# Kernel optimization log

Hardware: AMD Instinct MI355X
Metric: run time of the kernel (lower is better)

The kernel has to match this reference:

```python
import jax, jax.numpy as jnp
import numpy as np
from jax import lax

B, FC, TC, HID, HR, G, H, W = 4, 64, 64, 48, 2, 8, 128, 256
D = 2 * HR + 1          # 5 disparity offsets
CG = FC // G            # channels per correlation group
GRU_IN = TC + 2 * FC + 4 + G * D  # 236


def conv2d(x, w, b=None, pad=0):
    y = lax.conv_general_dilated(x, w, (1, 1), [(pad, pad), (pad, pad)],
                                 dimension_numbers=('NCHW', 'OIHW', 'NCHW'))
    return y if b is None else y + b[None, :, None, None]


def group_norm(x, scale, bias, groups=8, eps=1e-5):
    Bn, C, Hh, Ww = x.shape
    xg = x.reshape(Bn, groups, -1)
    m = jnp.mean(xg, -1, keepdims=True)
    v = jnp.var(xg, -1, keepdims=True)
    xg = (xg - m) * lax.rsqrt(v + eps)
    return xg.reshape(Bn, C, Hh, Ww) * scale[None, :, None, None] + bias[None, :, None, None]


def hsample(f, x):
    """grid_sample(align_corners=True, padding_mode='border') specialized to
    horizontal-only displacement: gy hits exact rows so only width is interpolated.
    f: [B,C,H,W], x: [B,H,W] source x-coords (unnormalized)."""
    Wf = f.shape[-1]
    xc = jnp.clip(x, 0.0, Wf - 1)          # border padding clamps coordinate
    x0 = jnp.floor(xc)
    w1 = xc - x0
    i0 = x0.astype(jnp.int32)
    i1 = jnp.minimum(i0 + 1, Wf - 1)
    i0b = jnp.broadcast_to(i0[:, None], f.shape)
    i1b = jnp.broadcast_to(i1[:, None], f.shape)
    f0 = jnp.take_along_axis(f, i0b, axis=-1)
    f1 = jnp.take_along_axis(f, i1b, axis=-1)
    return f0 * (1.0 - w1)[:, None] + f1 * w1[:, None]


def _forward(d, sx, sy, conf, feat, fL, fR,
             conv_z_w, conv_z_b, conv_r_w, conv_r_b, conv_q_w, conv_q_b,
             trunk1_w, gn1_s, gn1_b, trunk2_w, gn2_s, gn2_b,
             head_d_w, head_d_b, head_sx_w, head_sx_b,
             head_sy_w, head_sy_b, head_conf_w, head_conf_b):
    Bn, C, Hh, Ww = fL.shape
    xx = jnp.arange(Ww, dtype=fL.dtype)
    d0 = d[:, 0]                                     # [B,H,W]

    # horizontal warp of right features at current disparity
    fR_w = hsample(fR, xx[None, None, :] - d0)       # [B,C,H,W]

    # correlation lookup over D offsets around d (vectorized over D)
    d_off = jnp.arange(D, dtype=fL.dtype) - HR       # [D]
    xs = xx[None, None, None, :] - (d0[:, None] + d_off[None, :, None, None])  # [B,D,H,W]
    samp = jax.vmap(lambda xd: hsample(fR, xd), in_axes=1, out_axes=1)(xs)     # [B,D,C,H,W]
    fL_g = fL.reshape(Bn, G, CG, Hh, Ww)
    fR_g = samp.reshape(Bn, D, G, CG, Hh, Ww)
    cost = jnp.einsum('bgchw,bdgchw->bgdhw', fL_g, fR_g) / CG  # mean over cg
    cost = cost.reshape(Bn, G * D, Hh, Ww)

    ctx = jnp.concatenate([fL, fR_w, d, sx, sy, conf, cost], axis=1)
    hctx = jnp.concatenate([feat, ctx], axis=1)
    z = jax.nn.sigmoid(conv2d(hctx, conv_z_w, conv_z_b, pad=1))
    r = jax.nn.sigmoid(conv2d(hctx, conv_r_w, conv_r_b, pad=1))
    q = jnp.tanh(conv2d(jnp.concatenate([r * feat, ctx], axis=1), conv_q_w, conv_q_b, pad=1))
    h_new = (1.0 - z) * feat + z * q

    t = jax.nn.silu(group_norm(conv2d(h_new, trunk1_w, pad=1), gn1_s, gn1_b))
    t = jax.nn.silu(group_norm(conv2d(t, trunk2_w, pad=1), gn2_s, gn2_b))

    d_out = jax.nn.softplus(conv2d(t, head_d_w, head_d_b) + d)
    sx_out = sx + conv2d(t, head_sx_w, head_sx_b) * 0.1
    sy_out = sy + conv2d(t, head_sy_w, head_sy_b) * 0.1
    conf_out = jax.nn.sigmoid(conv2d(t, head_conf_w, head_conf_b) + 2.0 * conf - 1.0)
    return d_out, sx_out, sy_out, h_new, conf_out


def setup_inputs() -> dict:
    key = jax.random.key(0)
    ks = jax.random.split(key, 24)
    s = 0.02  # weight scale so gates/tanh stay in sensitive range
    return {
        'd': jax.random.uniform(ks[0], (B, 1, H, W), jnp.float32) * 32.0,
        'sx': jax.random.normal(ks[1], (B, 1, H, W), jnp.float32) * 0.1,
        'sy': jax.random.normal(ks[2], (B, 1, H, W), jnp.float32) * 0.1,
        'conf': jax.random.uniform(ks[3], (B, 1, H, W), jnp.float32),
        'feat': jax.random.normal(ks[4], (B, TC, H, W), jnp.float32),
        'fL': jax.random.normal(ks[5], (B, FC, H, W), jnp.float32),
        'fR': jax.random.normal(ks[6], (B, FC, H, W), jnp.float32),
        'conv_z_w': jax.random.normal(ks[7], (TC, GRU_IN, 3, 3), jnp.float32) * s,
        'conv_z_b': jnp.zeros((TC,), jnp.float32),
        'conv_r_w': jax.random.normal(ks[8], (TC, GRU_IN, 3, 3), jnp.float32) * s,
        'conv_r_b': jnp.zeros((TC,), jnp.float32),
        'conv_q_w': jax.random.normal(ks[9], (TC, GRU_IN, 3, 3), jnp.float32) * s,
        'conv_q_b': jnp.zeros((TC,), jnp.float32),
        'trunk1_w': jax.random.normal(ks[10], (HID, TC, 3, 3), jnp.float32) * s,
        'gn1_s': jnp.ones((HID,), jnp.float32),
        'gn1_b': jnp.zeros((HID,), jnp.float32),
        'trunk2_w': jax.random.normal(ks[11], (HID, HID, 3, 3), jnp.float32) * s,
        'gn2_s': jnp.ones((HID,), jnp.float32),
        'gn2_b': jnp.zeros((HID,), jnp.float32),
        'head_d_w': jax.random.normal(ks[12], (1, HID, 1, 1), jnp.float32) * s,
        'head_d_b': jnp.zeros((1,), jnp.float32),
        'head_sx_w': jax.random.normal(ks[13], (1, HID, 1, 1), jnp.float32) * s,
        'head_sx_b': jnp.zeros((1,), jnp.float32),
        'head_sy_w': jax.random.normal(ks[14], (1, HID, 1, 1), jnp.float32) * s,
        'head_sy_b': jnp.zeros((1,), jnp.float32),
        'head_conf_w': jax.random.normal(ks[15], (1, HID, 1, 1), jnp.float32) * s,
        'head_conf_b': jnp.zeros((1,), jnp.float32),
    }


def reference(d, sx, sy, conf, feat, fL, fR,
              conv_z_w, conv_z_b, conv_r_w, conv_r_b, conv_q_w, conv_q_b,
              trunk1_w, gn1_s, gn1_b, trunk2_w, gn2_s, gn2_b,
              head_d_w, head_d_b, head_sx_w, head_sx_b,
              head_sy_w, head_sy_b, head_conf_w, head_conf_b):
    return _forward(d, sx, sy, conf, feat, fL, fR,
                    conv_z_w, conv_z_b, conv_r_w, conv_r_b, conv_q_w, conv_q_b,
                    trunk1_w, gn1_s, gn1_b, trunk2_w, gn2_s, gn2_b,
                    head_d_w, head_d_b, head_sx_w, head_sx_b,
                    head_sy_w, head_sy_b, head_conf_w, head_conf_b)
```

## Files before the change

kernel.cpp:

```cpp
#include <hip/hip_runtime.h>
#include <hip/hip_bf16.h>
#include <math.h>
#include <type_traits>

typedef __hip_bfloat16 bf16;
typedef __attribute__((ext_vector_type(8))) short bf16x8;
typedef __attribute__((ext_vector_type(4))) float f32x4;

#define B_    4
#define H_    128
#define W_    256
#define HW_   32768
#define CTXC  172
#define NPIX  131072
#define RW    258
#define RH    130
#define IPX   33540

__device__ __forceinline__ float b2f(bf16 v) { return __bfloat162float(v); }
__device__ __forceinline__ bf16  f2b(float v){ return __float2bfloat16(v); }
__device__ __forceinline__ unsigned short f2bu(float v){ bf16 h = f2b(v); return *(unsigned short*)&h; }
__device__ __forceinline__ float ldv(const float* p){ return *p; }
__device__ __forceinline__ float ldv(const bf16* p) { return b2f(*p); }

__global__ void detect_k(const unsigned int* __restrict__ feat_raw,
                         int* __restrict__ flag)
{
    if (threadIdx.x != 0 || blockIdx.x != 0) return;
    int hits = 0;
    for (int i = 0; i < 64; ++i) {
        unsigned int w = feat_raw[i];
        unsigned int e = (w >> 7) & 0xFFu;
        hits += (e >= 0xC0u) ? 1 : 0;
    }
    *flag = (hits > 0) ? 1 : 0;
}

template<typename IT>
__device__ __forceinline__ bool gate_skip(const int* flag)
{
    constexpr bool isf = std::is_same<IT, float>::value;
    return (*flag != 0) != isf;
}

template<typename IT>
__global__ __launch_bounds__(256) void wfrag_gru(const int* __restrict__ flag,
                                                 const IT* __restrict__ src,
                                                 bf16* __restrict__ dst)
{
    if (gate_skip<IT>(flag)) return;
    int i = blockIdx.x * 256 + threadIdx.x;
    if (i >= 9*8*4*64*8) return;
    int j    = i & 7;
    int lane = (i >> 3) & 63;
    int u    = (i >> 9) & 3;
    int s    = (i >> 11) & 7;
    int t    = i >> 14;
    int klocal = ((lane >> 4) << 3) + j;
    int co = u * 16 + (lane & 15);
    float v = 0.f;
    if (s < 6) {
        int k = s * 32 + klocal;
        if (k < CTXC) v = ldv(src + ((size_t)co * 236 + 64 + k) * 9 + t);
    } else {
        int kf = (s - 6) * 32 + klocal;
        v = ldv(src + ((size_t)co * 236 + kf) * 9 + t);
    }
    dst[i] = f2b(v);
}

template<typename IT>
__global__ __launch_bounds__(256) void wfrag_trunk(const int* __restrict__ flag,
                                                   const IT* __restrict__ src,
                                                   bf16* __restrict__ dst, int CIN)
{
    if (gate_skip<IT>(flag)) return;
    int i = blockIdx.x * 256 + threadIdx.x;
    if (i >= 9*2*3*64*8) return;
    int j    = i & 7;
    int lane = (i >> 3) & 63;
    int rest = i >> 9;
    int u = rest % 3; rest /= 3;
    int s = rest & 1;
    int t = rest >> 1;
    int k = s * 32 + ((lane >> 4) << 3) + j;
    int co = u * 16 + (lane & 15);
    float v = (k < CIN) ? ldv(src + ((size_t)co * CIN + k) * 9 + t) : 0.f;
    dst[i] = f2b(v);
}

template<typename IT>
__global__ void cvt_small(const int* __restrict__ flag,
    const IT* zb, const IT* rb, const IT* qb,
    const IT* g1s, const IT* g1b, const IT* g2s, const IT* g2b,
    const IT* wd, const IT* wx, const IT* wy, const IT* wc,
    const IT* bd, const IT* bx, const IT* by, const IT* bc,
    bf16* __restrict__ dst)
{
    if (gate_skip<IT>(flag)) return;
    int i = blockIdx.x * 256 + threadIdx.x;
    if (i >= 580) return;
    const IT* src; int off;
    if      (i < 64)  { src = zb;  off = i; }
    else if (i < 128) { src = rb;  off = i - 64; }
    else if (i < 192) { src = qb;  off = i - 128; }
    else if (i < 240) { src = g1s; off = i - 192; }
    else if (i < 288) { src = g1b; off = i - 240; }
    else if (i < 336) { src = g2s; off = i - 288; }
    else if (i < 384) { src = g2b; off = i - 336; }
    else if (i < 432) { src = wd;  off = i - 384; }
    else if (i < 480) { src = wx;  off = i - 432; }
    else if (i < 528) { src = wy;  off = i - 480; }
    else if (i < 576) { src = wc;  off = i - 528; }
    else if (i == 576){ src = bd;  off = 0; }
    else if (i == 577){ src = bx;  off = 0; }
    else if (i == 578){ src = by;  off = 0; }
    else              { src = bc;  off = 0; }
    dst[i] = f2b(ldv(src + off));
}

template<typename IT>
__global__ __launch_bounds__(256) void build_ctx_nhwc(
    const int* __restrict__ flag,
    const IT* __restrict__ d_, const IT* __restrict__ sx_,
    const IT* __restrict__ sy_, const IT* __restrict__ conf_,
    const IT* __restrict__ fL, const IT* __restrict__ fR,
    const IT* __restrict__ feat,
    bf16* __restrict__ xin, float* __restrict__ dscf)
{
    if (gate_skip<IT>(flag)) return;
    const int x   = threadIdx.x;
    const int y   = blockIdx.x & (H_ - 1);
    const int b   = blockIdx.x >> 7;
    const int pix = (b << 15) | (y << 8) | x;

    const float d0 = ldv(d_ + pix);

    float xw = fminf(fmaxf((float)x - d0, 0.f), (float)(W_ - 1));
    float x0f = floorf(xw);
    float w1 = xw - x0f;
    int i0 = (int)x0f;
    int i1 = min(i0 + 1, W_ - 1);

    int   j0[5], j1[5];
    float wq[5];
#pragma unroll
    for (int dd = 0; dd < 5; ++dd) {
        float cd = fminf(fmaxf((float)x - d0 - (float)(dd - 2), 0.f), (float)(W_ - 1));
        float c0 = floorf(cd);
        wq[dd] = cd - c0;
        j0[dd] = (int)c0;
        j1[dd] = min(j0[dd] + 1, W_ - 1);
    }

    float cost[40];
#pragma unroll
    for (int k = 0; k < 40; ++k) cost[k] = 0.f;

    const IT* fLrow = fL + (size_t)b * 64 * HW_ + y * W_;
    const IT* fRrow = fR + (size_t)b * 64 * HW_ + y * W_;
    bf16* rec = xin + ((size_t)(b * RH + y + 1) * RW + 1 + x) * 256;

    unsigned short bufL[8], bufW[8];
#pragma unroll
    for (int c = 0; c < 64; ++c) {
        const IT* fr = fRrow + (size_t)c * HW_;
        float fl = ldv(fLrow + (size_t)c * HW_ + x);
        float fw = ldv(fr + i0) * (1.f - w1) + ldv(fr + i1) * w1;
        bufL[c & 7] = f2bu(fl);
        bufW[c & 7] = f2bu(fw);
        const int g = c >> 3;
#pragma unroll
        for (int dd = 0; dd < 5; ++dd) {
            float s = ldv(fr + j0[dd]) * (1.f - wq[dd]) + ldv(fr + j1[dd]) * wq[dd];
            cost[g * 5 + dd] = fmaf(fl, s, cost[g * 5 + dd]);
        }
        if ((c & 7) == 7) {
            *(uint4*)(rec + (c - 7))      = *(uint4*)bufL;
            *(uint4*)(rec + 64 + (c - 7)) = *(uint4*)bufW;
        }
    }

    float sxv = ldv(sx_ + pix);
    float syv = ldv(sy_ + pix);
    float cfv = ldv(conf_ + pix);

    {
        unsigned short t8[8];
        t8[0] = f2bu(d0);  t8[1] = f2bu(sxv);
        t8[2] = f2bu(syv); t8[3] = f2bu(cfv);
#pragma unroll
        for (int k = 0; k < 4; ++k) t8[4 + k] = f2bu(cost[k] * 0.125f);
        *(uint4*)(rec + 128) = *(uint4*)t8;
#pragma unroll
        for (int ch = 1; ch < 6; ++ch) {
#pragma unroll
            for (int k = 0; k < 8; ++k) {
                int ci = ch * 8 - 4 + k;
                t8[k] = (ci < 40) ? f2bu(cost[ci] * 0.125f) : 0;
            }
            *(uint4*)(rec + 128 + ch * 8) = *(uint4*)t8;
        }
    }
    {
        uint4 z = {0u, 0u, 0u, 0u};
        *(uint4*)(rec + 176) = z;
        *(uint4*)(rec + 184) = z;
    }
    {
        const IT* fts = feat + (size_t)b * 64 * HW_ + y * W_ + x;
        unsigned short t8[8];
#pragma unroll
        for (int c = 0; c < 64; ++c) {
            t8[c & 7] = f2bu(ldv(fts + (size_t)c * HW_));
            if ((c & 7) == 7) *(uint4*)(rec + 192 + (c - 7)) = *(uint4*)t8;
        }
    }

    dscf[pix]            = d0;
    dscf[NPIX + pix]     = sxv;
    dscf[2 * NPIX + pix] = syv;
    dscf[3 * NPIX + pix] = cfv;
}

__global__ __launch_bounds__(256) void zero_halo(bf16* __restrict__ buf, int CP)
{
    int yy = blockIdx.x % RH;
    int b  = blockIdx.x / RH;
    for (int x = threadIdx.x; x < RW; x += 256) {
        bool h = (yy == 0) | (yy == RH - 1) | (x == 0) | (x == RW - 1);
        if (!h) continue;
        bf16* p = buf + ((size_t)(b * RH + yy) * RW + x) * CP;
        uint4 z = {0u, 0u, 0u, 0u};
        for (int c = 0; c < CP; c += 8)
            *(uint4*)(p + c) = z;
    }
}

__global__ __launch_bounds__(256) void zero_full(bf16* __restrict__ buf, int n16)
{
    int i = blockIdx.x * 256 + threadIdx.x;
    if (i >= n16) return;
    uint4 z = {0u, 0u, 0u, 0u};
    *(uint4*)(buf + (size_t)i * 8) = z;
}

template<int NCH, int NT, int MODE>
__global__ __launch_bounds__(256) void conv_tile(
    const bf16* __restrict__ srcA, const bf16* __restrict__ srcB,
    const bf16* __restrict__ wfrag, const bf16* __restrict__ bias,
    bf16* __restrict__ outn, int CPO,
    const bf16* __restrict__ xz,
    void* __restrict__ dout, const int* __restrict__ flag)
{
    constexpr int CPA = (NCH == 4) ? 256 : 64;
    __shared__ uint4 lds4[6 * 66 * 8];

    const int tid  = threadIdx.x;
    const int lane = tid & 63;
    const int wv   = tid >> 6;
    const int m    = lane & 15;
    const int quad = lane >> 4;

    const int bx = blockIdx.x;
    const int x0 = (bx & 3) << 6;
    const int y0 = ((bx >> 2) & 31) << 2;
    const int b  = bx >> 7;

    f32x4 acc[4][NT];
#pragma unroll
    for (int mt = 0; mt < 4; ++mt)
#pragma unroll
        for (int u = 0; u < NT; ++u)
            acc[mt][u] = (f32x4){0.f, 0.f, 0.f, 0.f};

    const size_t tileBase = (size_t)(b * RH + y0) * RW + x0;

    for (int ch = 0; ch < NCH; ++ch) {
        if (ch) __syncthreads();
        const bool useB = (MODE == 1) && (ch == 3);
        const bf16* gsrc = useB ? srcB : srcA;
        const int cpg  = useB ? 64 : CPA;
        const int cofs = useB ? 0 : ch * 64;
        for (int idx = tid; idx < 3168; idx += 256) {
            const int part = idx & 7;
            const int rp   = idx >> 3;
            const int rr   = rp / 66;
            const int cc   = rp - rr * 66;
            const uint4 v = *(const uint4*)(gsrc +
                (tileBase + (size_t)rr * RW + cc) * cpg + cofs + part * 8);
            lds4[rp * 8 + (part ^ (cc & 7))] = v;
        }
        __syncthreads();
#pragma unroll
        for (int t = 0; t < 9; ++t) {
            const int dy = t / 3, dx = t % 3;
#pragma unroll
            for (int s = 0; s < 2; ++s) {
                bf16x8 a[4];
#pragma unroll
                for (int mt = 0; mt < 4; ++mt) {
                    const int cc = mt * 16 + m + dx;
                    const int j  = (s * 4 + quad) ^ (cc & 7);
                    a[mt] = ((const bf16x8*)lds4)[((wv + dy) * 66 + cc) * 8 + j];
                }
#pragma unroll
                for (int u = 0; u < NT; ++u) {
                    bf16x8 bw = *(const bf16x8*)(wfrag +
                        ((size_t)(((t * (NCH * 2) + ch * 2 + s) * NT + u) * 64 + lane) << 3));
#pragma unroll
                    for (int mt = 0; mt < 4; ++mt)
                        acc[mt][u] = __builtin_amdgcn_mfma_f32_16x16x32_bf16(
                            a[mt], bw, acc[mt][u], 0, 0, 0);
                }
            }
        }
    }

    const int gy = y0 + wv;
    const size_t rec0 = (size_t)(b * RH + gy + 1) * RW + 1 + x0;
#pragma unroll
    for (int mt = 0; mt < 4; ++mt) {
        const int px0 = mt * 16 + quad * 4;
#pragma unroll
        for (int u = 0; u < NT; ++u) {
            const int n = u * 16 + m;
            if (MODE == 0) {
                float bn = b2f(bias[n]);
#pragma unroll
                for (int r = 0; r < 4; ++r) {
                    float v = acc[mt][u][r] + bn;
                    outn[(rec0 + px0 + r) * CPO + n] = f2b(1.f / (1.f + expf(-v)));
                }
            } else if (MODE == 3) {
                float bn = b2f(bias[n]);
#pragma unroll
                for (int r = 0; r < 4; ++r) {
                    float v = acc[mt][u][r] + bn;
                    float sg = 1.f / (1.f + expf(-v));
                    float fv = b2f(srcA[(rec0 + px0 + r) * 256 + 192 + n]);
                    outn[(rec0 + px0 + r) * CPO + n] = f2b(sg * fv);
                }
            } else if (MODE == 2) {
#pragma unroll
                for (int r = 0; r < 4; ++r)
                    outn[(rec0 + px0 + r) * CPO + n] = f2b(acc[mt][u][r]);
            } else {
                float bn = b2f(bias[n]);
                float hv[4];
#pragma unroll
                for (int r = 0; r < 4; ++r) {
                    float q = tanhf(acc[mt][u][r] + bn);
                    size_t ai = (rec0 + px0 + r) * 64 + n;
                    float zv = b2f(xz[ai]);
                    float fv = b2f(srcA[(rec0 + px0 + r) * 256 + 192 + n]);
                    hv[r] = (1.f - zv) * fv + zv * q;
                    outn[ai] = f2b(hv[r]);
                }
                size_t pb = ((size_t)(b * 64 + n) << 15) + gy * W_ + x0 + px0;
                if (*flag) {
                    float4 o; o.x = hv[0]; o.y = hv[1]; o.z = hv[2]; o.w = hv[3];
                    *(float4*)((float*)dout + 393216 + pb) = o;
                } else {
                    ushort4 o;
                    o.x = f2bu(hv[0]); o.y = f2bu(hv[1]);
                    o.z = f2bu(hv[2]); o.w = f2bu(hv[3]);
                    *(ushort4*)((bf16*)dout + 393216 + pb) = o;
                }
            }
        }
    }
}

__global__ __launch_bounds__(256) void gn_reduce_nhwc(const bf16* __restrict__ buf,
                                                      float* __restrict__ part, int CP)
{
    const int gp = blockIdx.x >> 3;
    const int pt = blockIdx.x & 7;
    const int b = gp >> 3, g = gp & 7;
    const int lo = pt * 4193;
    const int hi = min(lo + 4193, IPX);
    const bf16* base = buf + (size_t)b * IPX * CP + g * 6;
    float s = 0.f, ss = 0.f;
    for (int px = lo + threadIdx.x; px < hi; px += 256) {
        const bf16* q = base + (size_t)px * CP;
#pragma unroll
        for (int c = 0; c < 6; ++c) {
            float v = b2f(q[c]);
            s += v;
            ss = fmaf(v, v, ss);
        }
    }
#pragma unroll
    for (int o = 32; o > 0; o >>= 1) {
        s  += __shfl_down(s, o, 64);
        ss += __shfl_down(ss, o, 64);
    }
    __shared__ float sm[8];
    int wid = threadIdx.x >> 6;
    if ((threadIdx.x & 63) == 0) { sm[wid * 2] = s; sm[wid * 2 + 1] = ss; }
    __syncthreads();
    if (threadIdx.x == 0) {
        float S = 0.f, SS = 0.f;
        for (int i = 0; i < 4; ++i) { S += sm[i * 2]; SS += sm[i * 2 + 1]; }
        part[(gp * 8 + pt) * 2]     = S;
        part[(gp * 8 + pt) * 2 + 1] = SS;
    }
}

__global__ void gn_finalize(const float* __restrict__ part, float* __restrict__ stats)
{
    int gp = threadIdx.x;
    if (gp >= 32) return;
    float S = 0.f, SS = 0.f;
    for (int i = 0; i < 8; ++i) {
        S  += part[(gp * 8 + i) * 2];
        SS += part[(gp * 8 + i) * 2 + 1];
    }
    const float N = 6.f * HW_;
    float mn  = S / N;
    float var = SS / N - mn * mn;
    var = fmaxf(var, 0.f);
    stats[gp * 2]     = mn;
    stats[gp * 2 + 1] = rsqrtf(var + 1e-5f);
}

__global__ __launch_bounds__(256) void gn_apply_nhwc(bf16* __restrict__ buf,
                                                     const float* __restrict__ stats,
                                                     const bf16* __restrict__ scbi,
                                                     int CP)
{
    const int y = blockIdx.x & (H_ - 1);
    const int b = blockIdx.x >> 7;
    bf16* base = buf + ((size_t)(b * RH + y + 1) * RW + 1) * CP;
    for (int j = threadIdx.x; j < W_ * 48; j += 256) {
        int px = j / 48;
        int c  = j - px * 48;
        int g  = c / 6;
        float mn = stats[(b * 8 + g) * 2], rr = stats[(b * 8 + g) * 2 + 1];
        size_t idx = (size_t)px * CP + c;
        float v = (b2f(base[idx]) - mn) * rr * b2f(scbi[c]) + b2f(scbi[48 + c]);
        base[idx] = f2b(v / (1.f + expf(-v)));
    }
}

__global__ __launch_bounds__(256) void heads_k(
    const bf16* __restrict__ xt2,
    const bf16* __restrict__ sp,
    const float* __restrict__ dscf,
    void* __restrict__ out_base,
    const int* __restrict__ flag)
{
    const int x = threadIdx.x;
    const int y = blockIdx.x & (H_ - 1);
    const int b = blockIdx.x >> 7;
    const int pix = (b << 15) | (y << 8) | x;
    const bf16* t = xt2 + ((size_t)(b * RH + y + 1) * RW + 1 + x) * 48;
    float ad = 0.f, ax = 0.f, ay = 0.f, ac = 0.f;
#pragma unroll
    for (int c = 0; c < 48; ++c) {
        float v = b2f(t[c]);
        ad = fmaf(v, b2f(sp[384 + c]), ad);
        ax = fmaf(v, b2f(sp[432 + c]), ax);
        ay = fmaf(v, b2f(sp[480 + c]), ay);
        ac = fmaf(v, b2f(sp[528 + c]), ac);
    }
    float dv  = dscf[pix];
    float sxv = dscf[NPIX + pix];
    float syv = dscf[2 * NPIX + pix];
    float cfv = dscf[3 * NPIX + pix];

    float dval = ad + b2f(sp[576]) + dv;
    float spv = fmaxf(dval, 0.f) + log1pf(expf(-fabsf(dval)));
    float sxo = sxv + 0.1f * (ax + b2f(sp[577]));
    float syo = syv + 0.1f * (ay + b2f(sp[578]));
    float cvv = 1.f / (1.f + expf(-(ac + b2f(sp[579]) + 2.f * cfv - 1.f)));

    if (*flag) {
        float* of = (float*)out_base;
        of[pix]            = spv;
        of[NPIX + pix]     = sxo;
        of[2 * NPIX + pix] = syo;
        of[8781824 + pix]  = cvv;
    } else {
        bf16* ob = (bf16*)out_base;
        ob[pix]            = f2b(spv);
        ob[NPIX + pix]     = f2b(sxo);
        ob[2 * NPIX + pix] = f2b(syo);
        ob[8781824 + pix]  = f2b(cvv);
    }
}

extern "C" void kernel_launch(void* const* d_in, const int* in_sizes, int n_in,
                              void* d_out, int out_size, void* d_ws, size_t ws_size,
                              hipStream_t stream)
{
    char* ws = (char*)d_ws;
    size_t off = 0;
    bf16* xin = (bf16*)(ws + off); off += (size_t)B_ * IPX * 256 * 2;
    bf16* xz  = (bf16*)(ws + off); off += (size_t)B_ * IPX * 64 * 2;
    bf16* xr  = (bf16*)(ws + off); off += (size_t)B_ * IPX * 64 * 2;
    bf16* xt  = (bf16*)(ws + off); off += (size_t)B_ * IPX * 64 * 2;
    bf16* xt1 = xz;
    bf16* xt2 = xr;
    float* dscf = (float*)(ws + off); off += (size_t)4 * NPIX * 4;
    bf16* wfz = (bf16*)(ws + off); off += 9*8*4*64*8 * 2;
    bf16* wfr = (bf16*)(ws + off); off += 9*8*4*64*8 * 2;
    bf16* wfq = (bf16*)(ws + off); off += 9*8*4*64*8 * 2;
    bf16* wf1 = (bf16*)(ws + off); off += 9*2*3*64*8 * 2;
    bf16* wf2 = (bf16*)(ws + off); off += 9*2*3*64*8 * 2;
    bf16*  sprm  = (bf16*)(ws + off); off += 1536;
    float* gpart = (float*)(ws + off); off += 512 * 4;
    float* gstat = (float*)(ws + off); off += 64 * 4;
    int*   flag  = (int*)(ws + off);   off += 256;

    detect_k<<<1, 64, 0, stream>>>((const unsigned int*)d_in[4], flag);

    wfrag_gru<bf16 ><<<576, 256, 0, stream>>>(flag, (const bf16*)d_in[7],  wfz);
    wfrag_gru<float><<<576, 256, 0, stream>>>(flag, (const float*)d_in[7], wfz);
    wfrag_gru<bf16 ><<<576, 256, 0, stream>>>(flag, (const bf16*)d_in[9],  wfr);
    wfrag_gru<float><<<576, 256, 0, stream>>>(flag, (const float*)d_in[9], wfr);
    wfrag_gru<bf16 ><<<576, 256, 0, stream>>>(flag, (const bf16*)d_in[11],  wfq);
    wfrag_gru<float><<<576, 256, 0, stream>>>(flag, (const float*)d_in[11], wfq);
    wfrag_trunk<bf16 ><<<108, 256, 0, stream>>>(flag, (const bf16*)d_in[13],  wf1, 64);
    wfrag_trunk<float><<<108, 256, 0, stream>>>(flag, (const float*)d_in[13], wf1, 64);
    wfrag_trunk<bf16 ><<<108, 256, 0, stream>>>(flag, (const bf16*)d_in[16],  wf2, 48);
    wfrag_trunk<float><<<108, 256, 0, stream>>>(flag, (const float*)d_in[16], wf2, 48);
    cvt_small<bf16><<<3, 256, 0, stream>>>(flag,
        (const bf16*)d_in[8], (const bf16*)d_in[10], (const bf16*)d_in[12],
        (const bf16*)d_in[14], (const bf16*)d_in[15], (const bf16*)d_in[17], (const bf16*)d_in[18],
        (const bf16*)d_in[19], (const bf16*)d_in[21], (const bf16*)d_in[23], (const bf16*)d_in[25],
        (const bf16*)d_in[20], (const bf16*)d_in[22], (const bf16*)d_in[24], (const bf16*)d_in[26],
        sprm);
    cvt_small<float><<<3, 256, 0, stream>>>(flag,
        (const float*)d_in[8], (const float*)d_in[10], (const float*)d_in[12],
        (const float*)d_in[14], (const float*)d_in[15], (const float*)d_in[17], (const float*)d_in[18],
        (const float*)d_in[19], (const float*)d_in[21], (const float*)d_in[23], (const float*)d_in[25],
        (const float*)d_in[20], (const float*)d_in[22], (const float*)d_in[24], (const float*)d_in[26],
        sprm);

    zero_halo<<<B_ * RH, 256, 0, stream>>>(xin, 256);
    zero_halo<<<B_ * RH, 256, 0, stream>>>(xr, 64);
    zero_halo<<<B_ * RH, 256, 0, stream>>>(xt, 64);
    build_ctx_nhwc<bf16 ><<<B_ * H_, 256, 0, stream>>>(flag,
        (const bf16*)d_in[0], (const bf16*)d_in[1], (const bf16*)d_in[2],
        (const bf16*)d_in[3], (const bf16*)d_in[5], (const bf16*)d_in[6],
        (const bf16*)d_in[4], xin, dscf);
    build_ctx_nhwc<float><<<B_ * H_, 256, 0, stream>>>(flag,
        (const float*)d_in[0], (const float*)d_in[1], (const float*)d_in[2],
        (const float*)d_in[3], (const float*)d_in[5], (const float*)d_in[6],
        (const float*)d_in[4], xin, dscf);

    conv_tile<4, 4, 0><<<512, 256, 0, stream>>>(xin, nullptr, wfz, sprm + 0,
        xz, 64, nullptr, nullptr, flag);
    conv_tile<4, 4, 3><<<512, 256, 0, stream>>>(xin, nullptr, wfr, sprm + 64,
        xr, 64, nullptr, nullptr, flag);
    conv_tile<4, 4, 1><<<512, 256, 0, stream>>>(xin, xr, wfq, sprm + 128,
        xt, 64, xz, d_out, flag);

    zero_full<<<(B_ * IPX * 64 / 8 + 255) / 256, 256, 0, stream>>>(xt1, B_ * IPX * 64 / 8);
    zero_halo<<<B_ * RH, 256, 0, stream>>>(xt2, 48);
    conv_tile<1, 3, 2><<<512, 256, 0, stream>>>(xt, nullptr, wf1, sprm,
        xt1, 64, nullptr, nullptr, flag);
    gn_reduce_nhwc<<<256, 256, 0, stream>>>(xt1, gpart, 64);
    gn_finalize<<<1, 32, 0, stream>>>(gpart, gstat);
    gn_apply_nhwc<<<B_ * H_, 256, 0, stream>>>(xt1, gstat, sprm + 192, 64);

    conv_tile<1, 3, 2><<<512, 256, 0, stream>>>(xt1, nullptr, wf2, sprm,
        xt2, 48, nullptr, nullptr, flag);
    gn_reduce_nhwc<<<256, 256, 0, stream>>>(xt2, gpart, 48);
    gn_finalize<<<1, 32, 0, stream>>>(gpart, gstat);
    gn_apply_nhwc<<<B_ * H_, 256, 0, stream>>>(xt2, gstat, sprm + 288, 48);

    heads_k<<<B_ * H_, 256, 0, stream>>>(xt2, sprm, dscf, d_out, flag);
}
```

Measured before the change: 646.0 us.

## Fuse z and r gate convolutions and split context build across channel groups

The z and r GRU gate convolutions now run as one conv_tile pass with 8 output tiles over an interleaved weight-fragment buffer. This reads the 256-channel input once instead of twice and saves a kernel launch. build_ctx_nhwc now launches four times as many blocks, each thread handling 16 channels plus a 64-pixel slice, and uses a shared-window fast path for the five correlation samples when the sample position is away from the borders. In exchange, the fused conv carries double the accumulators, which raises register pressure and may reduce occupancy.

```diff
diff --git a/kernel.cpp b/kernel.cpp
--- a/kernel.cpp
+++ b/kernel.cpp
@@ -46,7 +46,8 @@
 template<typename IT>
 __global__ __launch_bounds__(256) void wfrag_gru(const int* __restrict__ flag,
                                                  const IT* __restrict__ src,
-                                                 bf16* __restrict__ dst)
+                                                 bf16* __restrict__ dst,
+                                                 int NTtot, int ubase)
 {
     if (gate_skip<IT>(flag)) return;
     int i = blockIdx.x * 256 + threadIdx.x;
@@ -66,7 +67,7 @@
         int kf = (s - 6) * 32 + klocal;
         v = ldv(src + ((size_t)co * 236 + kf) * 9 + t);
     }
-    dst[i] = f2b(v);
+    dst[(((size_t)(t * 8 + s) * NTtot + ubase + u) * 64 + lane) * 8 + j] = f2b(v);
 }
 
 template<typename IT>
@@ -129,98 +130,108 @@
     bf16* __restrict__ xin, float* __restrict__ dscf)
 {
     if (gate_skip<IT>(flag)) return;
-    const int x   = threadIdx.x;
-    const int y   = blockIdx.x & (H_ - 1);
-    const int b   = blockIdx.x >> 7;
-    const int pix = (b << 15) | (y << 8) | x;
-
-    const float d0 = ldv(d_ + pix);
-
-    float xw = fminf(fmaxf((float)x - d0, 0.f), (float)(W_ - 1));
-    float x0f = floorf(xw);
-    float w1 = xw - x0f;
-    int i0 = (int)x0f;
-    int i1 = min(i0 + 1, W_ - 1);
+    const int lane = threadIdx.x & 63;
+    const int g2   = threadIdx.x >> 6;
+    const int blk  = blockIdx.x;
+    const int x    = ((blk & 3) << 6) | lane;
+    const int y    = (blk >> 2) & (H_ - 1);
+    const int b    = blk >> 9;
+    const int pix  = (b << 15) | (y << 8) | x;
+
+    const float d0   = ldv(d_ + pix);
+    const float tpos = (float)x - d0;
+    const float xw   = fminf(fmaxf(tpos, 0.f), 255.f);
+    const float x0f  = floorf(xw);
+    const float w1   = xw - x0f;
+    const int   i0   = (int)x0f;
+    const int   i1   = min(i0 + 1, W_ - 1);
+    const bool  safe = (tpos >= 2.f) && (tpos < 253.f);
+    const int   jb   = i0 - 2;
 
     int   j0[5], j1[5];
     float wq[5];
 #pragma unroll
     for (int dd = 0; dd < 5; ++dd) {
-        float cd = fminf(fmaxf((float)x - d0 - (float)(dd - 2), 0.f), (float)(W_ - 1));
+        float cd = fminf(fmaxf(tpos - (float)(dd - 2), 0.f), 255.f);
         float c0 = floorf(cd);
         wq[dd] = cd - c0;
         j0[dd] = (int)c0;
         j1[dd] = min(j0[dd] + 1, W_ - 1);
     }
 
-    float cost[40];
-#pragma unroll
-    for (int k = 0; k < 40; ++k) cost[k] = 0.f;
-
-    const IT* fLrow = fL + (size_t)b * 64 * HW_ + y * W_;
-    const IT* fRrow = fR + (size_t)b * 64 * HW_ + y * W_;
     bf16* rec = xin + ((size_t)(b * RH + y + 1) * RW + 1 + x) * 256;
-
-    unsigned short bufL[8], bufW[8];
-#pragma unroll
-    for (int c = 0; c < 64; ++c) {
-        const IT* fr = fRrow + (size_t)c * HW_;
-        float fl = ldv(fLrow + (size_t)c * HW_ + x);
-        float fw = ldv(fr + i0) * (1.f - w1) + ldv(fr + i1) * w1;
-        bufL[c & 7] = f2bu(fl);
-        bufW[c & 7] = f2bu(fw);
-        const int g = c >> 3;
-#pragma unroll
-        for (int dd = 0; dd < 5; ++dd) {
-            float s = ldv(fr + j0[dd]) * (1.f - wq[dd]) + ldv(fr + j1[dd]) * wq[dd];
-            cost[g * 5 + dd] = fmaf(fl, s, cost[g * 5 + dd]);
+    const IT* fLr = fL   + (size_t)(b * 64 + (g2 << 4)) * HW_ + y * W_;
+    const IT* fRr = fR   + (size_t)(b * 64 + (g2 << 4)) * HW_ + y * W_;
+    const IT* fTr = feat + (size_t)(b * 64 + (g2 << 4)) * HW_ + y * W_;
+
+    float cost[10];
+#pragma unroll
+    for (int k = 0; k < 10; ++k) cost[k] = 0.f;
+
+    unsigned short bL[8], bW[8], bF[8];
+#pragma unroll
+    for (int cc = 0; cc < 16; ++cc) {
+        const IT* fr = fRr + (size_t)cc * HW_;
+        float fl = ldv(fLr + (size_t)cc * HW_ + x);
+        float ft = ldv(fTr + (size_t)cc * HW_ + x);
+        float fw, s0, s1, s3, s4;
+        if (safe) {
+            float v0 = ldv(fr + jb),     v1 = ldv(fr + jb + 1);
+            float v2 = ldv(fr + jb + 2), v3 = ldv(fr + jb + 3);
+            float v4 = ldv(fr + jb + 4), v5 = ldv(fr + jb + 5);
+            float a = 1.f - w1;
+            fw = v2 * a + v3 * w1;
+            s0 = v4 * a + v5 * w1;
+            s1 = v3 * a + v4 * w1;
+            s3 = v1 * a + v2 * w1;
+            s4 = v0 * a + v1 * w1;
+        } else {
+            fw = ldv(fr + i0) * (1.f - w1) + ldv(fr + i1) * w1;
+            s0 = ldv(fr + j0[0]) * (1.f - wq[0]) + ldv(fr + j1[0]) * wq[0];
+            s1 = ldv(fr + j0[1]) * (1.f - wq[1]) + ldv(fr + j1[1]) * wq[1];
+            s3 = ldv(fr + j0[3]) * (1.f - wq[3]) + ldv(fr + j1[3]) * wq[3];
+            s4 = ldv(fr + j0[4]) * (1.f - wq[4]) + ldv(fr + j1[4]) * wq[4];
         }
-        if ((c & 7) == 7) {
-            *(uint4*)(rec + (c - 7))      = *(uint4*)bufL;
-            *(uint4*)(rec + 64 + (c - 7)) = *(uint4*)bufW;
+        const int gg = cc >> 3;
+        cost[gg * 5 + 0] = fmaf(fl, s0, cost[gg * 5 + 0]);
+        cost[gg * 5 + 1] = fmaf(fl, s1, cost[gg * 5 + 1]);
+        cost[gg * 5 + 2] = fmaf(fl, fw, cost[gg * 5 + 2]);
+        cost[gg * 5 + 3] = fmaf(fl, s3, cost[gg * 5 + 3]);
+        cost[gg * 5 + 4] = fmaf(fl, s4, cost[gg * 5 + 4]);
+        bL[cc & 7] = f2bu(fl);
+        bW[cc & 7] = f2bu(fw);
+        bF[cc & 7] = f2bu(ft);
+        if ((cc & 7) == 7) {
+            const int c0i = (g2 << 4) + cc - 7;
+            *(uint4*)(rec + c0i)       = *(uint4*)bL;
+            *(uint4*)(rec + 64 + c0i)  = *(uint4*)bW;
+            *(uint4*)(rec + 192 + c0i) = *(uint4*)bF;
         }
     }
 
-    float sxv = ldv(sx_ + pix);
-    float syv = ldv(sy_ + pix);
-    float cfv = ldv(conf_ + pix);
-
-    {
-        unsigned short t8[8];
-        t8[0] = f2bu(d0);  t8[1] = f2bu(sxv);
-        t8[2] = f2bu(syv); t8[3] = f2bu(cfv);
-#pragma unroll
-        for (int k = 0; k < 4; ++k) t8[4 + k] = f2bu(cost[k] * 0.125f);
-        *(uint4*)(rec + 128) = *(uint4*)t8;
-#pragma unroll
-        for (int ch = 1; ch < 6; ++ch) {
-#pragma unroll
-            for (int k = 0; k < 8; ++k) {
-                int ci = ch * 8 - 4 + k;
-                t8[k] = (ci < 40) ? f2bu(cost[ci] * 0.125f) : 0;
-            }
-            *(uint4*)(rec + 128 + ch * 8) = *(uint4*)t8;
-        }
-    }
-    {
-        uint4 z = {0u, 0u, 0u, 0u};
-        *(uint4*)(rec + 176) = z;
-        *(uint4*)(rec + 184) = z;
-    }
-    {
-        const IT* fts = feat + (size_t)b * 64 * HW_ + y * W_ + x;
-        unsigned short t8[8];
-#pragma unroll
-        for (int c = 0; c < 64; ++c) {
-            t8[c & 7] = f2bu(ldv(fts + (size_t)c * HW_));
-            if ((c & 7) == 7) *(uint4*)(rec + 192 + (c - 7)) = *(uint4*)t8;
-        }
-    }
-
-    dscf[pix]            = d0;
-    dscf[NPIX + pix]     = sxv;
-    dscf[2 * NPIX + pix] = syv;
-    dscf[3 * NPIX + pix] = cfv;
+    bf16* cst = rec + 132 + g2 * 10;
+#pragma unroll
+    for (int k = 0; k < 5; ++k) {
+        unsigned int pk = (unsigned int)f2bu(cost[2 * k] * 0.125f) |
+                          ((unsigned int)f2bu(cost[2 * k + 1] * 0.125f) << 16);
+        *(unsigned int*)(cst + 2 * k) = pk;
+    }
+
+    if (g2 == 0) {
+        float sxv = ldv(sx_ + pix);
+        float syv = ldv(sy_ + pix);
+        float cfv = ldv(conf_ + pix);
+        *(unsigned int*)(rec + 128) = (unsigned int)f2bu(d0)  | ((unsigned int)f2bu(sxv) << 16);
+        *(unsigned int*)(rec + 130) = (unsigned int)f2bu(syv) | ((unsigned int)f2bu(cfv) << 16);
+        dscf[pix]            = d0;
+        dscf[NPIX + pix]     = sxv;
+        dscf[2 * NPIX + pix] = syv;
+        dscf[3 * NPIX + pix] = cfv;
+    } else if (g2 == 3) {
+#pragma unroll
+        for (int k = 0; k < 10; ++k)
+            *(unsigned int*)(rec + 172 + 2 * k) = 0u;
+    }
 }
 
 __global__ __launch_bounds__(256) void zero_halo(bf16* __restrict__ buf, int CP)
@@ -250,7 +261,7 @@
     const bf16* __restrict__ srcA, const bf16* __restrict__ srcB,
     const bf16* __restrict__ wfrag, const bf16* __restrict__ bias,
     bf16* __restrict__ outn, int CPO,
-    const bf16* __restrict__ xz,
+    bf16* __restrict__ o2,
     void* __restrict__ dout, const int* __restrict__ flag)
 {
     constexpr int CPA = (NCH == 4) ? 256 : 64;
@@ -324,35 +335,34 @@
         const int px0 = mt * 16 + quad * 4;
 #pragma unroll
         for (int u = 0; u < NT; ++u) {
-            const int n = u * 16 + m;
-            if (MODE == 0) {
-                float bn = b2f(bias[n]);
-#pragma unroll
-                for (int r = 0; r < 4; ++r) {
-                    float v = acc[mt][u][r] + bn;
-                    outn[(rec0 + px0 + r) * CPO + n] = f2b(1.f / (1.f + expf(-v)));
-                }
-            } else if (MODE == 3) {
-                float bn = b2f(bias[n]);
+            if (MODE == 4) {
+                const int n = (u & 3) * 16 + m;
+                float bn = b2f(bias[(u < 4 ? 0 : 64) + n]);
 #pragma unroll
                 for (int r = 0; r < 4; ++r) {
                     float v = acc[mt][u][r] + bn;
                     float sg = 1.f / (1.f + expf(-v));
-                    float fv = b2f(srcA[(rec0 + px0 + r) * 256 + 192 + n]);
-                    outn[(rec0 + px0 + r) * CPO + n] = f2b(sg * fv);
+                    if (u < 4) {
+                        outn[(rec0 + px0 + r) * 64 + n] = f2b(sg);
+                    } else {
+                        float fv = b2f(srcA[(rec0 + px0 + r) * 256 + 192 + n]);
+                        o2[(rec0 + px0 + r) * 64 + n] = f2b(sg * fv);
+                    }
                 }
             } else if (MODE == 2) {
+                const int n = u * 16 + m;
 #pragma unroll
                 for (int r = 0; r < 4; ++r)
                     outn[(rec0 + px0 + r) * CPO + n] = f2b(acc[mt][u][r]);
-            } else {
+            } else if (MODE == 1) {
+                const int n = u * 16 + m;
                 float bn = b2f(bias[n]);
                 float hv[4];
 #pragma unroll
                 for (int r = 0; r < 4; ++r) {
                     float q = tanhf(acc[mt][u][r] + bn);
                     size_t ai = (rec0 + px0 + r) * 64 + n;
-                    float zv = b2f(xz[ai]);
+                    float zv = b2f(o2[ai]);
                     float fv = b2f(srcA[(rec0 + px0 + r) * 256 + 192 + n]);
                     hv[r] = (1.f - zv) * fv + zv * q;
                     outn[ai] = f2b(hv[r]);
@@ -504,11 +514,10 @@
     bf16* xt1 = xz;
     bf16* xt2 = xr;
     float* dscf = (float*)(ws + off); off += (size_t)4 * NPIX * 4;
-    bf16* wfz = (bf16*)(ws + off); off += 9*8*4*64*8 * 2;
-    bf16* wfr = (bf16*)(ws + off); off += 9*8*4*64*8 * 2;
-    bf16* wfq = (bf16*)(ws + off); off += 9*8*4*64*8 * 2;
-    bf16* wf1 = (bf16*)(ws + off); off += 9*2*3*64*8 * 2;
-    bf16* wf2 = (bf16*)(ws + off); off += 9*2*3*64*8 * 2;
+    bf16* wfzr = (bf16*)(ws + off); off += (size_t)9*8*8*64*8 * 2;
+    bf16* wfq  = (bf16*)(ws + off); off += (size_t)9*8*4*64*8 * 2;
+    bf16* wf1  = (bf16*)(ws + off); off += (size_t)9*2*3*64*8 * 2;
+    bf16* wf2  = (bf16*)(ws + off); off += (size_t)9*2*3*64*8 * 2;
     bf16*  sprm  = (bf16*)(ws + off); off += 1536;
     float* gpart = (float*)(ws + off); off += 512 * 4;
     float* gstat = (float*)(ws + off); off += 64 * 4;
@@ -516,12 +525,12 @@
 
     detect_k<<<1, 64, 0, stream>>>((const unsigned int*)d_in[4], flag);
 
-    wfrag_gru<bf16 ><<<576, 256, 0, stream>>>(flag, (const bf16*)d_in[7],  wfz);
-    wfrag_gru<float><<<576, 256, 0, stream>>>(flag, (const float*)d_in[7], wfz);
-    wfrag_gru<bf16 ><<<576, 256, 0, stream>>>(flag, (const bf16*)d_in[9],  wfr);
-    wfrag_gru<float><<<576, 256, 0, stream>>>(flag, (const float*)d_in[9], wfr);
-    wfrag_gru<bf16 ><<<576, 256, 0, stream>>>(flag, (const bf16*)d_in[11],  wfq);
-    wfrag_gru<float><<<576, 256, 0, stream>>>(flag, (const float*)d_in[11], wfq);
+    wfrag_gru<bf16 ><<<576, 256, 0, stream>>>(flag, (const bf16*)d_in[7],  wfzr, 8, 0);
+    wfrag_gru<float><<<576, 256, 0, stream>>>(flag, (const float*)d_in[7], wfzr, 8, 0);
+    wfrag_gru<bf16 ><<<576, 256, 0, stream>>>(flag, (const bf16*)d_in[9],  wfzr, 8, 4);
+    wfrag_gru<float><<<576, 256, 0, stream>>>(flag, (const float*)d_in[9], wfzr, 8, 4);
+    wfrag_gru<bf16 ><<<576, 256, 0, stream>>>(flag, (const bf16*)d_in[11],  wfq, 4, 0);
+    wfrag_gru<float><<<576, 256, 0, stream>>>(flag, (const float*)d_in[11], wfq, 4, 0);
     wfrag_trunk<bf16 ><<<108, 256, 0, stream>>>(flag, (const bf16*)d_in[13],  wf1, 64);
     wfrag_trunk<float><<<108, 256, 0, stream>>>(flag, (const float*)d_in[13], wf1, 64);
     wfrag_trunk<bf16 ><<<108, 256, 0, stream>>>(flag, (const bf16*)d_in[16],  wf2, 48);
@@ -542,19 +551,17 @@
     zero_halo<<<B_ * RH, 256, 0, stream>>>(xin, 256);
     zero_halo<<<B_ * RH, 256, 0, stream>>>(xr, 64);
     zero_halo<<<B_ * RH, 256, 0, stream>>>(xt, 64);
-    build_ctx_nhwc<bf16 ><<<B_ * H_, 256, 0, stream>>>(flag,
+    build_ctx_nhwc<bf16 ><<<B_ * H_ * 4, 256, 0, stream>>>(flag,
         (const bf16*)d_in[0], (const bf16*)d_in[1], (const bf16*)d_in[2],
         (const bf16*)d_in[3], (const bf16*)d_in[5], (const bf16*)d_in[6],
         (const bf16*)d_in[4], xin, dscf);
-    build_ctx_nhwc<float><<<B_ * H_, 256, 0, stream>>>(flag,
+    build_ctx_nhwc<float><<<B_ * H_ * 4, 256, 0, stream>>>(flag,
         (const float*)d_in[0], (const float*)d_in[1], (const float*)d_in[2],
         (const float*)d_in[3], (const float*)d_in[5], (const float*)d_in[6],
         (const float*)d_in[4], xin, dscf);
 
-    conv_tile<4, 4, 0><<<512, 256, 0, stream>>>(xin, nullptr, wfz, sprm + 0,
-        xz, 64, nullptr, nullptr, flag);
-    conv_tile<4, 4, 3><<<512, 256, 0, stream>>>(xin, nullptr, wfr, sprm + 64,
-        xr, 64, nullptr, nullptr, flag);
+    conv_tile<4, 8, 4><<<512, 256, 0, stream>>>(xin, nullptr, wfzr, sprm,
+        xz, 64, xr, nullptr, flag);
     conv_tile<4, 4, 1><<<512, 256, 0, stream>>>(xin, xr, wfq, sprm + 128,
         xt, 64, xz, d_out, flag);
 
```

Result: slower. 892.3 us (+38.1%).
